# Kernel tuning notes

Measured on AMD Instinct MI355X. Metric: run time of the kernel, lower is better.

## Reference

```python
import jax, jax.numpy as jnp
import numpy as np

N, D, H = 8192, 512, 512

def setup_inputs() -> dict:
    key = jax.random.key(0)
    ks = jax.random.split(key, 9)
    s_in = 1.0 / np.sqrt(D)
    s_h = 1.0 / np.sqrt(H)
    return {
        "x": jax.random.normal(ks[0], (N, D), jnp.float32),
        "Wq": jax.random.uniform(ks[1], (D, H), jnp.float32, -s_in, s_in),
        "bq": jax.random.uniform(ks[2], (H,), jnp.float32, -s_in, s_in),
        "Wk": jax.random.uniform(ks[3], (D, H), jnp.float32, -s_in, s_in),
        "bk": jax.random.uniform(ks[4], (H,), jnp.float32, -s_in, s_in),
        "Wv": jax.random.uniform(ks[5], (D, H), jnp.float32, -s_in, s_in),
        "bv": jax.random.uniform(ks[6], (H,), jnp.float32, -s_in, s_in),
        "Wo": jax.random.uniform(ks[7], (H, H), jnp.float32, -s_h, s_h),
        "bo": jax.random.uniform(ks[8], (H,), jnp.float32, -s_h, s_h),
    }

def reference(x, Wq, bq, Wk, bk, Wv, bv, Wo, bo):
    q = x @ Wq + bq            # [N, H]
    k = x @ Wk + bk            # [N, H]
    v = x @ Wv + bv            # [N, H]
    scores = (q @ k.T) * (1.0 / jnp.sqrt(jnp.asarray(H, q.dtype)))  # [N, N]
    attn = jax.nn.softmax(scores, axis=-1)
    attended = attn @ v        # [N, H]
    return attended @ Wo + bo  # [N, H]
```

## Files before the change

### kernel.cpp

```cpp
#include <hip/hip_runtime.h>

typedef short sh8 __attribute__((ext_vector_type(8)));
typedef float f32x4 __attribute__((ext_vector_type(4)));

#define DEV __device__ __forceinline__

DEV f32x4 mfma16(sh8 a, sh8 b, f32x4 c) {
  return __builtin_amdgcn_mfma_f32_16x16x32_bf16(a, b, c, 0, 0, 0);
}

DEV unsigned short f2bf(float f) {
  unsigned u = __float_as_uint(f);
  u = u + 0x7FFFu + ((u >> 16) & 1u);
  return (unsigned short)(u >> 16);
}

DEV unsigned cvtpk(float lo, float hi) {
  unsigned r;
  asm("v_cvt_pk_bf16_f32 %0, %1, %2" : "=v"(r) : "v"(lo), "v"(hi));
  return r;
}

DEV void gll16(const void* g, void* l) {
  __builtin_amdgcn_global_load_lds(
      (const __attribute__((address_space(1))) unsigned int*)g,
      (__attribute__((address_space(3))) unsigned int*)l, 16, 0, 0);
}

__global__ void cvt_x_kernel(const float* __restrict__ x, unsigned short* __restrict__ xb, int n4) {
  int i = blockIdx.x * blockDim.x + threadIdx.x;
  int stride = gridDim.x * blockDim.x;
  for (; i < n4; i += stride) {
    float4 v = ((const float4*)x)[i];
    ushort4 o;
    o.x = f2bf(v.x); o.y = f2bf(v.y); o.z = f2bf(v.z); o.w = f2bf(v.w);
    ((ushort4*)xb)[i] = o;
  }
}

__global__ void cvt_wT_kernel(const float* __restrict__ W0, const float* __restrict__ W1,
                              const float* __restrict__ W2, const float* __restrict__ W3,
                              unsigned short* __restrict__ T0, unsigned short* __restrict__ T1,
                              unsigned short* __restrict__ T2, unsigned short* __restrict__ T3) {
  const float* W; unsigned short* T;
  switch (blockIdx.z) {
    case 0: W = W0; T = T0; break;
    case 1: W = W1; T = T1; break;
    case 2: W = W2; T = T2; break;
    default: W = W3; T = T3; break;
  }
  __shared__ float tile[32][33];
  int tx = threadIdx.x & 31, ty = threadIdx.x >> 5;
  int r0 = blockIdx.y * 32, c0 = blockIdx.x * 32;
#pragma unroll
  for (int i = 0; i < 4; i++) tile[ty + i * 8][tx] = W[(r0 + ty + i * 8) * 512 + c0 + tx];
  __syncthreads();
#pragma unroll
  for (int i = 0; i < 4; i++) T[(c0 + ty + i * 8) * 512 + r0 + tx] = f2bf(tile[tx][ty + i * 8]);
}

__global__ __launch_bounds__(512, 2) void gemm256_u_kernel(
    const unsigned short* __restrict__ Q, const unsigned short* __restrict__ Kb,
    unsigned short* __restrict__ U, float* __restrict__ lpart) {
  __shared__ __align__(16) unsigned short smem[65536];
  const int tid = threadIdx.x, lane = tid & 63;
  const int w = tid >> 6;
  const int g = lane >> 4, r = lane & 15;
  const int wm2 = w & 1, wn4 = w >> 1;
  const int wgid = (blockIdx.x & 7) * 128 + (blockIdx.x >> 3);
  const int brow = (wgid >> 5) * 256;
  const int bcol = (wgid & 31) * 256;
  const int srow = tid >> 3;
  const int sg = tid & 7;

  f32x4 acc[2][2][4][2] = {};

#define STG(b, a, h, kt)                                                                       \
  do {                                                                                         \
    const unsigned short* _src = (a) ? Kb : Q;                                                 \
    int _base = (a) ? bcol : brow;                                                             \
    int _r0 = (h) * 128 + srow;                                                                \
    int _r1 = _r0 + 64;                                                                        \
    unsigned short* _d = smem + (b) * 32768 + (a) * 16384 + (h) * 8192 + tid * 8;              \
    gll16(_src + (size_t)(_base + _r0) * 512 + (kt) * 64 + ((sg ^ (_r0 & 7)) * 8), _d);        \
    gll16(_src + (size_t)(_base + _r1) * 512 + (kt) * 64 + ((sg ^ (_r1 & 7)) * 8), _d + 4096); \
  } while (0)

  auto LDK = [&](sh8 (&kf)[2][4], int B_, int kh) {
    const unsigned short* Bs = smem + B_ * 32768 + 16384;
#pragma unroll
    for (int kk = 0; kk < 2; kk++)
#pragma unroll
      for (int m = 0; m < 4; m++) {
        int row = kh * 128 + wm2 * 64 + m * 16 + r;
        kf[kk][m] = *(const sh8*)&Bs[row * 64 + (((kk * 4 + g) ^ (r & 7)) * 8)];
      }
  };
  auto LDQ = [&](sh8 (&qf)[2][2], int B_, int qh) {
    const unsigned short* As = smem + B_ * 32768;
#pragma unroll
    for (int kk = 0; kk < 2; kk++)
#pragma unroll
      for (int n = 0; n < 2; n++) {
        int row = qh * 128 + wn4 * 32 + n * 16 + r;
        qf[kk][n] = *(const sh8*)&As[row * 64 + (((kk * 4 + g) ^ (r & 7)) * 8)];
      }
  };
  auto MM = [&](f32x4 (&c)[4][2], sh8 (&kf)[2][4], sh8 (&qf)[2][2]) {
    __builtin_amdgcn_s_setprio(1);
#pragma unroll
    for (int kk = 0; kk < 2; kk++)
#pragma unroll
      for (int m = 0; m < 4; m++)
#pragma unroll
        for (int n = 0; n < 2; n++)
          c[m][n] = mfma16(kf[kk][m], qf[kk][n], c[m][n]);
    __builtin_amdgcn_s_setprio(0);
  };
#define BAR asm volatile("s_barrier" ::: "memory")
#define VM2 asm volatile("s_waitcnt vmcnt(2)" ::: "memory")

  STG(0, 0, 0, 0); STG(0, 0, 1, 0); STG(0, 1, 0, 0); STG(0, 1, 1, 0);
  asm volatile("s_waitcnt vmcnt(0)" ::: "memory");
  BAR;

#pragma unroll
  for (int kt = 0; kt < 8; ++kt) {
    const int cur = kt & 1, nb = cur ^ 1;
    const int kn = (kt < 7) ? kt + 1 : 7;
    sh8 k0[2][4], k1[2][4], q0[2][2], q1[2][2];
    LDK(k0, cur, 0); LDQ(q0, cur, 0);
    STG(nb, 0, 0, kn);
    VM2; BAR;
    MM(acc[0][0], k0, q0);
    BAR;
    LDQ(q1, cur, 1);
    STG(nb, 0, 1, kn);
    BAR;
    MM(acc[0][1], k0, q1);
    BAR;
    LDK(k1, cur, 1);
    STG(nb, 1, 0, kn);
    BAR;
    MM(acc[1][0], k1, q0);
    BAR;
    STG(nb, 1, 1, kn);
    VM2; BAR;
    MM(acc[1][1], k1, q1);
    BAR;
  }
#undef STG
#undef BAR
#undef VM2

  asm volatile("s_waitcnt vmcnt(0)" ::: "memory");
  __syncthreads();

  const float K2c = 0.04419417382415922f * 1.4426950408889634f;
#pragma unroll
  for (int qh = 0; qh < 2; qh++)
#pragma unroll
    for (int n = 0; n < 2; n++) {
      int qr = qh * 128 + wn4 * 32 + n * 16 + r;
      float s = 0.f;
#pragma unroll
      for (int kh = 0; kh < 2; kh++)
#pragma unroll
        for (int m = 0; m < 4; m++) {
          f32x4 a = acc[kh][qh][m][n];
          float v0 = __builtin_amdgcn_exp2f(a[0] * K2c);
          float v1 = __builtin_amdgcn_exp2f(a[1] * K2c);
          float v2 = __builtin_amdgcn_exp2f(a[2] * K2c);
          float v3 = __builtin_amdgcn_exp2f(a[3] * K2c);
          s += (v0 + v1) + (v2 + v3);
          uint2 pk; pk.x = cvtpk(v0, v1); pk.y = cvtpk(v2, v3);
          int ke = kh * 128 + wm2 * 64 + m * 16 + g * 4;
          int el = qr * 256 + (ke ^ ((qr & 7) * 8));
          *(uint2*)&smem[el] = pk;
        }
      s += __shfl_xor(s, 16);
      s += __shfl_xor(s, 32);
      if (g == 0)
        lpart[(size_t)((bcol >> 7) + wm2) * 8192 + brow + qr] = s;
    }
  __syncthreads();
#pragma unroll
  for (int jj = 0; jj < 16; jj++) {
    int row = jj * 16 + (tid >> 5);
    int g32 = tid & 31;
    uint4 v = *(const uint4*)&smem[row * 256 + ((g32 ^ (row & 7)) * 8)];
    *(uint4*)&U[(size_t)(brow + row) * 8192 + bcol + g32 * 8] = v;
  }
}

template <int MODE>
DEV void gemm_core(const unsigned short* __restrict__ A, int lda,
                   const unsigned short* __restrict__ Bt, int ldb,
                   const float* __restrict__ bias, void* __restrict__ Cv, int ldc,
                   int kSteps, int koff, int brow, int bcol,
                   unsigned short* smem) {
  const int tid = threadIdx.x, lane = tid & 63, w = tid >> 6;
  const int g = lane >> 4, r = lane & 15;
  const int wr = w >> 1, wc = w & 1;
  const int rA = w * 8 + (lane >> 3);
  const int sgl = lane & 7;
  const int scol = ((sgl ^ (lane >> 3)) * 8);
  const unsigned short* aP = A + (size_t)(brow + rA) * lda + koff + scol;
  const unsigned short* bP = Bt + (size_t)(bcol + rA) * ldb + koff + scol;
  const int lOff = rA * 64 + sgl * 8;
  f32x4 acc[4][4] = {};
  const int fr = r & 7;

  auto STAGE = [&](int buf, int ks) {
    unsigned short* lA = smem + buf * 16384 + lOff;
    unsigned short* lB = smem + buf * 16384 + 8192 + lOff;
    const size_t ko = (size_t)ks * 64;
#pragma unroll
    for (int cc = 0; cc < 4; cc++) gll16(aP + (size_t)cc * 32 * lda + ko, lA + cc * 32 * 64);
#pragma unroll
    for (int cc = 0; cc < 4; cc++) gll16(bP + (size_t)cc * 32 * ldb + ko, lB + cc * 32 * 64);
  };
  auto COMPUTE = [&](int buf) {
    const unsigned short* As = smem + buf * 16384;
    const unsigned short* Bs = As + 8192;
#pragma unroll
    for (int kk = 0; kk < 2; kk++) {
      sh8 af[4], bfr[4];
#pragma unroll
      for (int m = 0; m < 4; m++)
        af[m] = *(const sh8*)&As[(wr * 64 + m * 16 + r) * 64 + (((kk * 4 + g) ^ fr) * 8)];
#pragma unroll
      for (int n = 0; n < 4; n++)
        bfr[n] = *(const sh8*)&Bs[(wc * 64 + n * 16 + r) * 64 + (((kk * 4 + g) ^ fr) * 8)];
#pragma unroll
      for (int m = 0; m < 4; m++)
#pragma unroll
        for (int n = 0; n < 4; n++) acc[m][n] = mfma16(af[m], bfr[n], acc[m][n]);
    }
  };

  STAGE(0, 0);
  int cur = 0;
  for (int ks = 0; ks + 1 < kSteps; ks++) {
    STAGE(cur ^ 1, ks + 1);
    asm volatile("s_waitcnt vmcnt(8)" ::: "memory");
    asm volatile("s_barrier" ::: "memory");
    COMPUTE(cur);
    asm volatile("s_barrier" ::: "memory");
    cur ^= 1;
  }
  asm volatile("s_waitcnt vmcnt(0)" ::: "memory");
  asm volatile("s_barrier" ::: "memory");
  COMPUTE(cur);

  if (MODE == 0) {
#pragma unroll
    for (int n = 0; n < 4; n++) {
      int col = bcol + wc * 64 + n * 16 + r;
      float bv = bias ? bias[col] : 0.f;
#pragma unroll
      for (int m = 0; m < 4; m++) {
        int row = brow + wr * 64 + m * 16 + g * 4;
#pragma unroll
        for (int i = 0; i < 4; i++)
          ((float*)Cv)[(size_t)(row + i) * ldc + col] = acc[m][n][i] + bv;
      }
    }
  } else {
    __syncthreads();
#pragma unroll
    for (int m = 0; m < 4; m++) {
#pragma unroll
      for (int n = 0; n < 4; n++) {
        int coll = wc * 64 + n * 16 + r;
        float bv = bias ? bias[bcol + coll] : 0.f;
        int rb = (wr * 64 + m * 16 + g * 4) * 132 + coll;
        smem[rb] = f2bf(acc[m][n][0] + bv);
        smem[rb + 132] = f2bf(acc[m][n][1] + bv);
        smem[rb + 264] = f2bf(acc[m][n][2] + bv);
        smem[rb + 396] = f2bf(acc[m][n][3] + bv);
      }
    }
    __syncthreads();
    unsigned short* C = (unsigned short*)Cv;
#pragma unroll
    for (int j = 0; j < 8; j++) {
      int row = w * 32 + j * 4 + (lane >> 4);
      int colb = (lane & 15) * 8;
      uint4 v = *(const uint4*)&smem[row * 132 + colb];
      *(uint4*)&C[(size_t)(brow + row) * ldc + bcol + colb] = v;
    }
  }
}

__global__ __launch_bounds__(256, 2) void gemm_qkv_kernel(
    const unsigned short* __restrict__ A,
    const unsigned short* __restrict__ B0, const unsigned short* __restrict__ B1,
    const unsigned short* __restrict__ B2,
    const float* __restrict__ c0, const float* __restrict__ c1, const float* __restrict__ c2,
    unsigned short* __restrict__ C0, unsigned short* __restrict__ C1,
    unsigned short* __restrict__ C2) {
  __shared__ __align__(16) unsigned short smem[32768];
  const unsigned short* Bt; const float* bias; unsigned short* C;
  switch (blockIdx.z) {
    case 0: Bt = B0; bias = c0; C = C0; break;
    case 1: Bt = B1; bias = c1; C = C1; break;
    default: Bt = B2; bias = c2; C = C2; break;
  }
  gemm_core<1>(A, 512, Bt, 512, bias, C, 512, 8, 0,
               blockIdx.x * 128, blockIdx.y * 128, smem);
}

__global__ __launch_bounds__(256, 2) void gemm_pv_kernel(
    const unsigned short* __restrict__ U, const unsigned short* __restrict__ VT,
    float* __restrict__ P0, float* __restrict__ P1) {
  __shared__ __align__(16) unsigned short smem[32768];
  const int b = blockIdx.x;
  const int c = b & 7, xt = c & 3, zt = c >> 2, yt = b >> 3;
  float* P = zt ? P1 : P0;
  gemm_core<0>(U, 8192, VT, 8192, nullptr, P, 512, 64, zt * 4096,
               yt * 128, xt * 128, smem);
}

__global__ __launch_bounds__(256, 2) void gemm_o_kernel(
    const unsigned short* __restrict__ att, const unsigned short* __restrict__ woT,
    const float* __restrict__ bo, float* __restrict__ out) {
  __shared__ __align__(16) unsigned short smem[32768];
  gemm_core<0>(att, 512, woT, 512, bo, out, 512, 8, 0,
               blockIdx.x * 128, blockIdx.y * 128, smem);
}

__global__ void transpose_v_kernel(const unsigned short* __restrict__ in, unsigned short* __restrict__ out) {
  __shared__ unsigned short tile[32][33];
  int tx = threadIdx.x & 31, ty = threadIdx.x >> 5;
  int r0 = blockIdx.y * 32, c0 = blockIdx.x * 32;
#pragma unroll
  for (int i = 0; i < 4; i++) tile[ty + i * 8][tx] = in[(size_t)(r0 + ty + i * 8) * 512 + c0 + tx];
  __syncthreads();
#pragma unroll
  for (int i = 0; i < 4; i++) out[(size_t)(c0 + ty + i * 8) * 8192 + r0 + tx] = tile[tx][ty + i * 8];
}

__global__ void combine_l_kernel(const float* __restrict__ lpart, float* __restrict__ linv) {
  int row = blockIdx.x * 256 + threadIdx.x;
  float s = 0.f;
#pragma unroll 8
  for (int j = 0; j < 64; j++) s += lpart[(size_t)j * 8192 + row];
  linv[row] = 1.0f / s;
}

__global__ void addcvt_kernel(const float* __restrict__ a, const float* __restrict__ b,
                              const float* __restrict__ linv,
                              unsigned short* __restrict__ o, int n4) {
  int i = blockIdx.x * blockDim.x + threadIdx.x;
  int stride = gridDim.x * blockDim.x;
  for (; i < n4; i += stride) {
    float inv = linv[i >> 7];
    float4 va = ((const float4*)a)[i];
    float4 vb = ((const float4*)b)[i];
    ushort4 ov;
    ov.x = f2bf((va.x + vb.x) * inv); ov.y = f2bf((va.y + vb.y) * inv);
    ov.z = f2bf((va.z + vb.z) * inv); ov.w = f2bf((va.w + vb.w) * inv);
    ((ushort4*)o)[i] = ov;
  }
}

extern "C" void kernel_launch(void* const* d_in, const int* in_sizes, int n_in,
                              void* d_out, int out_size, void* d_ws, size_t ws_size,
                              hipStream_t stream) {
  const float* x  = (const float*)d_in[0];
  const float* Wq = (const float*)d_in[1];
  const float* bq = (const float*)d_in[2];
  const float* Wk = (const float*)d_in[3];
  const float* bk = (const float*)d_in[4];
  const float* Wv = (const float*)d_in[5];
  const float* bv = (const float*)d_in[6];
  const float* Wo = (const float*)d_in[7];
  const float* bo = (const float*)d_in[8];
  char* ws = (char*)d_ws;

  unsigned short* U   = (unsigned short*)(ws + 0);
  unsigned short* xb  = (unsigned short*)(ws + 0);
  unsigned short* vb  = (unsigned short*)(ws + 8388608);
  unsigned short* att = (unsigned short*)(ws + 0);
  unsigned short* qb  = (unsigned short*)(ws + 134217728);
  unsigned short* kb  = (unsigned short*)(ws + 142606336);
  unsigned short* vtb = (unsigned short*)(ws + 150994944);
  unsigned short* wqT = (unsigned short*)(ws + 159383552);
  unsigned short* wkT = (unsigned short*)(ws + 159907840);
  unsigned short* wvT = (unsigned short*)(ws + 160432128);
  unsigned short* woT = (unsigned short*)(ws + 160956416);
  float* lpart = (float*)(ws + 161480704);
  float* linv  = (float*)(ws + 165675008);
  float* P0 = (float*)qb;
  float* P1 = (float*)d_out;

  cvt_x_kernel<<<2048, 256, 0, stream>>>(x, xb, 8192 * 512 / 4);
  cvt_wT_kernel<<<dim3(16, 16, 4), 256, 0, stream>>>(Wq, Wk, Wv, Wo, wqT, wkT, wvT, woT);
  gemm_qkv_kernel<<<dim3(64, 4, 3), 256, 0, stream>>>(
      xb, wqT, wkT, wvT, bq, bk, bv, qb, kb, vb);
  transpose_v_kernel<<<dim3(16, 256), 256, 0, stream>>>(vb, vtb);
  gemm256_u_kernel<<<1024, 512, 0, stream>>>(qb, kb, U, lpart);
  combine_l_kernel<<<32, 256, 0, stream>>>(lpart, linv);
  gemm_pv_kernel<<<512, 256, 0, stream>>>(U, vtb, P0, P1);
  addcvt_kernel<<<2048, 256, 0, stream>>>(P0, P1, linv, att, 8192 * 512 / 4);
  gemm_o_kernel<<<dim3(64, 4), 256, 0, stream>>>(att, woT, bo, (float*)d_out);
}
```

Before: 234.0 us.

## Use 256x256-tile 512-thread PV GEMM with 4-way split-K bf16 partials

Replaces the 128x128 PV GEMM (2-way split-K, fp32 partials) with a dedicated 256x256-tile, 512-thread kernel modeled on the score kernel, splitting K four ways and writing bf16 partials. The reduce kernel now sums four bf16 partials and applies the softmax normalization. Larger tiles raise operand reuse from LDS and halve partial-sum traffic per element. The cost is lower precision in the partial sums and only 256 blocks, which may underfill the GPU's compute units.

```diff
diff --git a/kernel.cpp b/kernel.cpp
--- a/kernel.cpp
+++ b/kernel.cpp
@@ -150,8 +150,6 @@
     BAR;
   }
 #undef STG
-#undef BAR
-#undef VM2
 
   asm volatile("s_waitcnt vmcnt(0)" ::: "memory");
   __syncthreads();
@@ -190,6 +188,135 @@
     int g32 = tid & 31;
     uint4 v = *(const uint4*)&smem[row * 256 + ((g32 ^ (row & 7)) * 8)];
     *(uint4*)&U[(size_t)(brow + row) * 8192 + bcol + g32 * 8] = v;
+  }
+}
+
+__global__ __launch_bounds__(512, 2) void gemm256_pv_kernel(
+    const unsigned short* __restrict__ Uu, const unsigned short* __restrict__ VT,
+    unsigned short* __restrict__ P0, unsigned short* __restrict__ P1,
+    unsigned short* __restrict__ P2, unsigned short* __restrict__ P3) {
+  __shared__ __align__(16) unsigned short smem[65536];
+  const int tid = threadIdx.x, lane = tid & 63;
+  const int w = tid >> 6;
+  const int g = lane >> 4, r = lane & 15;
+  const int wm2 = w & 1, wn4 = w >> 1;
+  const int c = blockIdx.x & 7;
+  const int hi = blockIdx.x >> 3;
+  const int nt = hi & 1, qthi = hi >> 1;
+  const int qlo = c >> 2, kz = c & 3;
+  const int qt = qthi * 2 + qlo;
+  const int brow = qt * 256;
+  const int bcol = nt * 256;
+  const int koff = kz * 2048;
+  const int srow = tid >> 3;
+  const int sg = tid & 7;
+  unsigned short* P = (kz == 0) ? P0 : (kz == 1) ? P1 : (kz == 2) ? P2 : P3;
+
+  f32x4 acc[2][2][4][2] = {};
+
+#define STGP(b, a, h, kt)                                                                        \
+  do {                                                                                           \
+    const unsigned short* _src = (a) ? VT : Uu;                                                  \
+    int _base = (a) ? bcol : brow;                                                               \
+    int _r0 = (h) * 128 + srow;                                                                  \
+    int _r1 = _r0 + 64;                                                                          \
+    unsigned short* _d = smem + (b) * 32768 + (a) * 16384 + (h) * 8192 + tid * 8;                \
+    gll16(_src + (size_t)(_base + _r0) * 8192 + koff + (kt) * 64 + ((sg ^ (_r0 & 7)) * 8), _d);  \
+    gll16(_src + (size_t)(_base + _r1) * 8192 + koff + (kt) * 64 + ((sg ^ (_r1 & 7)) * 8),       \
+          _d + 4096);                                                                            \
+  } while (0)
+
+  auto LDV = [&](sh8 (&vf)[2][4], int B_, int dh) {
+    const unsigned short* Bs = smem + B_ * 32768 + 16384;
+#pragma unroll
+    for (int kk = 0; kk < 2; kk++)
+#pragma unroll
+      for (int m = 0; m < 4; m++) {
+        int row = dh * 128 + wm2 * 64 + m * 16 + r;
+        vf[kk][m] = *(const sh8*)&Bs[row * 64 + (((kk * 4 + g) ^ (r & 7)) * 8)];
+      }
+  };
+  auto LDU = [&](sh8 (&uf)[2][2], int B_, int qh) {
+    const unsigned short* As = smem + B_ * 32768;
+#pragma unroll
+    for (int kk = 0; kk < 2; kk++)
+#pragma unroll
+      for (int n = 0; n < 2; n++) {
+        int row = qh * 128 + wn4 * 32 + n * 16 + r;
+        uf[kk][n] = *(const sh8*)&As[row * 64 + (((kk * 4 + g) ^ (r & 7)) * 8)];
+      }
+  };
+  auto MM = [&](f32x4 (&cc)[4][2], sh8 (&vf)[2][4], sh8 (&uf)[2][2]) {
+    __builtin_amdgcn_s_setprio(1);
+#pragma unroll
+    for (int kk = 0; kk < 2; kk++)
+#pragma unroll
+      for (int m = 0; m < 4; m++)
+#pragma unroll
+        for (int n = 0; n < 2; n++)
+          cc[m][n] = mfma16(vf[kk][m], uf[kk][n], cc[m][n]);
+    __builtin_amdgcn_s_setprio(0);
+  };
+
+  STGP(0, 0, 0, 0); STGP(0, 0, 1, 0); STGP(0, 1, 0, 0); STGP(0, 1, 1, 0);
+  asm volatile("s_waitcnt vmcnt(0)" ::: "memory");
+  BAR;
+
+#pragma unroll 2
+  for (int kt = 0; kt < 32; ++kt) {
+    const int cur = kt & 1, nb = cur ^ 1;
+    const int kn = (kt < 31) ? kt + 1 : 31;
+    sh8 v0[2][4], v1[2][4], u0[2][2], u1[2][2];
+    LDV(v0, cur, 0); LDU(u0, cur, 0);
+    STGP(nb, 0, 0, kn);
+    VM2; BAR;
+    MM(acc[0][0], v0, u0);
+    BAR;
+    LDU(u1, cur, 1);
+    STGP(nb, 0, 1, kn);
+    BAR;
+    MM(acc[0][1], v0, u1);
+    BAR;
+    LDV(v1, cur, 1);
+    STGP(nb, 1, 0, kn);
+    BAR;
+    MM(acc[1][0], v1, u0);
+    BAR;
+    STGP(nb, 1, 1, kn);
+    VM2; BAR;
+    MM(acc[1][1], v1, u1);
+    BAR;
+  }
+#undef STGP
+#undef BAR
+#undef VM2
+
+  asm volatile("s_waitcnt vmcnt(0)" ::: "memory");
+  __syncthreads();
+
+#pragma unroll
+  for (int qh = 0; qh < 2; qh++)
+#pragma unroll
+    for (int n = 0; n < 2; n++) {
+      int qr = qh * 128 + wn4 * 32 + n * 16 + r;
+#pragma unroll
+      for (int dh = 0; dh < 2; dh++)
+#pragma unroll
+        for (int m = 0; m < 4; m++) {
+          f32x4 a = acc[dh][qh][m][n];
+          uint2 pk; pk.x = cvtpk(a[0], a[1]); pk.y = cvtpk(a[2], a[3]);
+          int de = dh * 128 + wm2 * 64 + m * 16 + g * 4;
+          int el = qr * 256 + (de ^ ((qr & 7) * 8));
+          *(uint2*)&smem[el] = pk;
+        }
+    }
+  __syncthreads();
+#pragma unroll
+  for (int jj = 0; jj < 16; jj++) {
+    int row = jj * 16 + (tid >> 5);
+    int g32 = tid & 31;
+    uint4 v = *(const uint4*)&smem[row * 256 + ((g32 ^ (row & 7)) * 8)];
+    *(uint4*)&P[(size_t)(brow + row) * 512 + bcol + g32 * 8] = v;
   }
 }
 
@@ -311,17 +438,6 @@
                blockIdx.x * 128, blockIdx.y * 128, smem);
 }
 
-__global__ __launch_bounds__(256, 2) void gemm_pv_kernel(
-    const unsigned short* __restrict__ U, const unsigned short* __restrict__ VT,
-    float* __restrict__ P0, float* __restrict__ P1) {
-  __shared__ __align__(16) unsigned short smem[32768];
-  const int b = blockIdx.x;
-  const int c = b & 7, xt = c & 3, zt = c >> 2, yt = b >> 3;
-  float* P = zt ? P1 : P0;
-  gemm_core<0>(U, 8192, VT, 8192, nullptr, P, 512, 64, zt * 4096,
-               yt * 128, xt * 128, smem);
-}
-
 __global__ __launch_bounds__(256, 2) void gemm_o_kernel(
     const unsigned short* __restrict__ att, const unsigned short* __restrict__ woT,
     const float* __restrict__ bo, float* __restrict__ out) {
@@ -349,19 +465,34 @@
   linv[row] = 1.0f / s;
 }
 
-__global__ void addcvt_kernel(const float* __restrict__ a, const float* __restrict__ b,
-                              const float* __restrict__ linv,
-                              unsigned short* __restrict__ o, int n4) {
+__global__ void addcvt4_kernel(const unsigned short* __restrict__ p0,
+                               const unsigned short* __restrict__ p1,
+                               const unsigned short* __restrict__ p2,
+                               const unsigned short* __restrict__ p3,
+                               const float* __restrict__ linv,
+                               unsigned short* __restrict__ o, int n8) {
   int i = blockIdx.x * blockDim.x + threadIdx.x;
   int stride = gridDim.x * blockDim.x;
-  for (; i < n4; i += stride) {
-    float inv = linv[i >> 7];
-    float4 va = ((const float4*)a)[i];
-    float4 vb = ((const float4*)b)[i];
-    ushort4 ov;
-    ov.x = f2bf((va.x + vb.x) * inv); ov.y = f2bf((va.y + vb.y) * inv);
-    ov.z = f2bf((va.z + vb.z) * inv); ov.w = f2bf((va.w + vb.w) * inv);
-    ((ushort4*)o)[i] = ov;
+  for (; i < n8; i += stride) {
+    float inv = linv[i >> 6];
+    uint4 a = ((const uint4*)p0)[i];
+    uint4 b = ((const uint4*)p1)[i];
+    uint4 c = ((const uint4*)p2)[i];
+    uint4 d = ((const uint4*)p3)[i];
+    const unsigned* ua = (const unsigned*)&a;
+    const unsigned* ub = (const unsigned*)&b;
+    const unsigned* uc = (const unsigned*)&c;
+    const unsigned* ud = (const unsigned*)&d;
+    unsigned out[4];
+#pragma unroll
+    for (int e = 0; e < 4; e++) {
+      float lo = __uint_as_float(ua[e] << 16) + __uint_as_float(ub[e] << 16) +
+                 __uint_as_float(uc[e] << 16) + __uint_as_float(ud[e] << 16);
+      float hi = __uint_as_float(ua[e] & 0xffff0000u) + __uint_as_float(ub[e] & 0xffff0000u) +
+                 __uint_as_float(uc[e] & 0xffff0000u) + __uint_as_float(ud[e] & 0xffff0000u);
+      out[e] = cvtpk(lo * inv, hi * inv);
+    }
+    ((uint4*)o)[i] = *(uint4*)out;
   }
 }
 
@@ -392,8 +523,10 @@
   unsigned short* woT = (unsigned short*)(ws + 160956416);
   float* lpart = (float*)(ws + 161480704);
   float* linv  = (float*)(ws + 165675008);
-  float* P0 = (float*)qb;
-  float* P1 = (float*)d_out;
+  unsigned short* P0 = qb;
+  unsigned short* P1 = kb;
+  unsigned short* P2 = (unsigned short*)d_out;
+  unsigned short* P3 = (unsigned short*)d_out + 4194304;
 
   cvt_x_kernel<<<2048, 256, 0, stream>>>(x, xb, 8192 * 512 / 4);
   cvt_wT_kernel<<<dim3(16, 16, 4), 256, 0, stream>>>(Wq, Wk, Wv, Wo, wqT, wkT, wvT, woT);
@@ -402,7 +535,7 @@
   transpose_v_kernel<<<dim3(16, 256), 256, 0, stream>>>(vb, vtb);
   gemm256_u_kernel<<<1024, 512, 0, stream>>>(qb, kb, U, lpart);
   combine_l_kernel<<<32, 256, 0, stream>>>(lpart, linv);
-  gemm_pv_kernel<<<512, 256, 0, stream>>>(U, vtb, P0, P1);
-  addcvt_kernel<<<2048, 256, 0, stream>>>(P0, P1, linv, att, 8192 * 512 / 4);
+  gemm256_pv_kernel<<<256, 512, 0, stream>>>(U, vtb, P0, P1, P2, P3);
+  addcvt4_kernel<<<2048, 256, 0, stream>>>(P0, P1, P2, P3, linv, att, 8192 * 512 / 8);
   gemm_o_kernel<<<dim3(64, 4), 256, 0, stream>>>(att, woT, bo, (float*)d_out);
 }
```

Result: faster. 211.6 us (-9.6%).
